# Kernel optimization log

Measured on AMD Instinct MI355X. Metric: run time of the kernel, lower is better.

## Reference

```python
import jax, jax.numpy as jnp
import numpy as np

LSTM_IN = 125
LSTM_H = 125
MLP_D_H = 512
N = 512


def _lstm_scan(x, Wih, Whh, bih, bhh):
    # x: (N, LSTM_IN); PyTorch gate order: i, f, g, o
    H = LSTM_H
    def step(carry, xt):
        h, c = carry
        g = Wih @ xt + Whh @ h + bih + bhh  # (4H,)
        i = jax.nn.sigmoid(g[:H])
        f = jax.nn.sigmoid(g[H:2 * H])
        gg = jnp.tanh(g[2 * H:3 * H])
        o = jax.nn.sigmoid(g[3 * H:])
        c = f * c + i * gg
        h = o * jnp.tanh(c)
        return (h, c), h
    init = (jnp.zeros((H,), x.dtype), jnp.zeros((H,), x.dtype))
    _, hs = jax.lax.scan(step, init, x)
    return hs  # (N, H)


def setup_inputs() -> dict:
    key = jax.random.key(0)
    ks = jax.random.split(key, 14)
    s = 0.05
    d = {
        "sentence_emb": jax.random.normal(ks[0], (N, 1, LSTM_IN), jnp.float32),
        "Wih_f": jax.random.normal(ks[1], (4 * LSTM_H, LSTM_IN), jnp.float32) * s,
        "Whh_f": jax.random.normal(ks[2], (4 * LSTM_H, LSTM_H), jnp.float32) * s,
        "bih_f": jax.random.normal(ks[3], (4 * LSTM_H,), jnp.float32) * s,
        "bhh_f": jax.random.normal(ks[4], (4 * LSTM_H,), jnp.float32) * s,
        "Wih_b": jax.random.normal(ks[5], (4 * LSTM_H, LSTM_IN), jnp.float32) * s,
        "Whh_b": jax.random.normal(ks[6], (4 * LSTM_H, LSTM_H), jnp.float32) * s,
        "bih_b": jax.random.normal(ks[7], (4 * LSTM_H,), jnp.float32) * s,
        "bhh_b": jax.random.normal(ks[8], (4 * LSTM_H,), jnp.float32) * s,
        "W1": jax.random.normal(ks[9], (MLP_D_H, 4 * LSTM_H), jnp.float32) * s,
        "b1": jax.random.normal(ks[10], (MLP_D_H,), jnp.float32) * s,
        "W2": jax.random.normal(ks[11], (1, MLP_D_H), jnp.float32) * s,
        "b2": jax.random.normal(ks[12], (1,), jnp.float32) * s,
    }
    return d


def reference(sentence_emb, Wih_f, Whh_f, bih_f, bhh_f, Wih_b, Whh_b, bih_b, bhh_b, W1, b1, W2, b2):
    x = sentence_emb[:, 0, :]  # (N, 125), batch=1
    h_fwd = _lstm_scan(x, Wih_f, Whh_f, bih_f, bhh_f)           # (N, 125)
    h_bwd = _lstm_scan(x[::-1], Wih_b, Whh_b, bih_b, bhh_b)[::-1]  # (N, 125)
    h = jnp.concatenate([h_fwd, h_bwd], axis=-1)  # (N, 250)
    # output_mtx[i, j] = MLP(concat(h[j], h[i]))
    # Decompose first linear: W1 @ cat(h_j, h_i) = Wa @ h_j + Wb @ h_i
    D = h.shape[-1]
    Pa = h @ W1[:, :D].T   # (N, H): contribution of h_j
    Pb = h @ W1[:, D:].T   # (N, H): contribution of h_i
    hidden = jnp.tanh(Pb[:, None, :] + Pa[None, :, :] + b1)  # (N, N, H)
    out = hidden @ W2[0] + b2[0]  # (N, N)
    return out
```

## Files before the change

kernel.cpp:

```cpp
#include <hip/hip_runtime.h>

typedef __bf16 bf16_t;
typedef __bf16 bf16x8 __attribute__((ext_vector_type(8)));
typedef float f32x4 __attribute__((ext_vector_type(4)));
typedef int   int4v __attribute__((ext_vector_type(4)));

#define LOG2E 1.4426950408889634f

template<int CTRL>
__device__ __forceinline__ float qperm(float x) {
  return __builtin_bit_cast(float,
      __builtin_amdgcn_update_dpp(0, __builtin_bit_cast(int, x), CTRL, 0xF, 0xF, true));
}

__device__ __forceinline__ void lds_barrier() {
  asm volatile("s_waitcnt lgkmcnt(0)\n\ts_barrier" ::: "memory");
}

__global__ __launch_bounds__(256) void pre_kernel(
    const float* __restrict__ x,
    const float* __restrict__ Wih_f, const float* __restrict__ bih_f,
    const float* __restrict__ bhh_f,
    const float* __restrict__ Wih_b, const float* __restrict__ bih_b,
    const float* __restrict__ bhh_b,
    float* __restrict__ preT)
{
  const int dir = blockIdx.x >> 5;
  const int T   = blockIdx.x & 31;
  const float* __restrict__ Wih = dir ? Wih_b : Wih_f;
  const float* __restrict__ bih = dir ? bih_b : bih_f;
  const float* __restrict__ bhh = dir ? bhh_b : bhh_f;

  const int tid = threadIdx.x;
  const int wv  = tid >> 6;
  const int lane = tid & 63;
  const int q = lane >> 4, cc = lane & 15;

  const int r  = 16 * T + cc;
  const int na = r >> 2, pa = r & 3;
  const bool vld = (na < 125);
  const float* __restrict__ Wr = Wih + (vld ? (125 * pa + na) * 125 : 0);

  bf16x8 whi[4], wlo[4];
  #pragma unroll
  for (int ks = 0; ks < 4; ++ks) {
    #pragma unroll
    for (int j = 0; j < 8; ++j) {
      int k = 32 * ks + 8 * q + j;
      float wvv = (vld && k < 125) ? Wr[k] : 0.0f;
      bf16_t hi = (bf16_t)wvv;
      whi[ks][j] = hi;
      wlo[ks][j] = (bf16_t)(wvv - (float)hi);
    }
  }

  float bias[4];
  #pragma unroll
  for (int reg = 0; reg < 4; ++reg) {
    int ro = 16 * T + 4 * q + reg;
    int no = ro >> 2, po = ro & 3;
    bias[reg] = (no < 125) ? (bih[125 * po + no] + bhh[125 * po + no]) : 0.0f;
  }

  for (int i = 0; i < 8; ++i) {
    const int tt = 8 * wv + i;
    const int t  = 16 * tt + cc;
    const int trow = dir ? (511 - t) : t;
    const float* __restrict__ xr = x + trow * 125;

    f32x4 acc = (f32x4)0.0f;
    #pragma unroll
    for (int ks = 0; ks < 4; ++ks) {
      bf16x8 xhi, xlo;
      #pragma unroll
      for (int j = 0; j < 8; ++j) {
        int k = 32 * ks + 8 * q + j;
        float xv = (k < 125) ? xr[k] : 0.0f;
        bf16_t hi = (bf16_t)xv;
        xhi[j] = hi;
        xlo[j] = (bf16_t)(xv - (float)hi);
      }
      acc = __builtin_amdgcn_mfma_f32_16x16x32_bf16(whi[ks], xhi, acc, 0, 0, 0);
      acc = __builtin_amdgcn_mfma_f32_16x16x32_bf16(whi[ks], xlo, acc, 0, 0, 0);
      acc = __builtin_amdgcn_mfma_f32_16x16x32_bf16(wlo[ks], xhi, acc, 0, 0, 0);
    }
    #pragma unroll
    for (int reg = 0; reg < 4; ++reg) {
      int ro = 16 * T + 4 * q + reg;
      preT[dir * 262144 + ro * 512 + 16 * tt + cc] = acc[reg] + bias[reg];
    }
  }
}

__global__ __launch_bounds__(512) void lstm_kernel(
    const float* __restrict__ Whh_f, const float* __restrict__ Whh_b,
    const float* __restrict__ pre,
    bf16_t* __restrict__ h_all)
{
  const int tid  = threadIdx.x;

  if (blockIdx.x >= 2) {
    const unsigned long long t0 = __builtin_amdgcn_s_memrealtime();
    float a = 1.0f + (float)tid;
    const float b = 1.0000001f;
    for (;;) {
      #pragma unroll
      for (int it = 0; it < 1024; ++it) a = fmaf(a, b, 1e-7f);
      if (__builtin_amdgcn_s_memrealtime() - t0 > 12000ull) break;
    }
    asm volatile("" :: "v"(a));
    return;
  }

  const int dir = blockIdx.x;
  const float* __restrict__ Whh = dir ? Whh_b : Whh_f;

  const int lane = tid & 63;
  const int w    = tid >> 6;
  const int q    = lane >> 4;
  const int cc   = lane & 15;
  const int lt   = cc >> 2;
  const int p    = cc & 3;

  float wm = 0.0f;
  #pragma unroll
  for (int LT = 0; LT < 4; ++LT) {
    int rr = 16 * (4 * w + LT) + cc;
    int nn = rr >> 2, pp = rr & 3;
    if (nn < 125) {
      const float* __restrict__ Wrow = Whh + (125 * pp + nn) * 125;
      #pragma unroll
      for (int ks = 0; ks < 2; ++ks)
        #pragma unroll
        for (int jj = 0; jj < 16; ++jj) {
          int k = 64 * ks + 16 * q + jj;
          if (k < 125) wm = fmaxf(wm, fabsf(Wrow[k]));
        }
    }
  }
  #pragma unroll
  for (int off = 1; off < 64; off <<= 1)
    wm = fmaxf(wm, __shfl_xor(wm, off));
  __shared__ float wmx[8];
  if (lane == 0) wmx[w] = wm;
  __syncthreads();
  float wmax = wmx[0];
  #pragma unroll
  for (int u = 1; u < 8; ++u) wmax = fmaxf(wmax, wmx[u]);
  const float s_w  = 127.0f / wmax;
  const float invq = wmax / (127.0f * 127.0f);

  int4v afrag[4][2];
  #pragma unroll
  for (int LT = 0; LT < 4; ++LT) {
    int rr = 16 * (4 * w + LT) + cc;
    int nn = rr >> 2, pp = rr & 3;
    bool avld = (nn < 125);
    const float* __restrict__ Wrow = Whh + (avld ? (125 * pp + nn) * 125 : 0);
    #pragma unroll
    for (int ks = 0; ks < 2; ++ks) {
      int4v v;
      #pragma unroll
      for (int word = 0; word < 4; ++word) {
        int b = 0;
        #pragma unroll
        for (int byte = 0; byte < 4; ++byte) {
          int jj = 4 * word + byte;
          int k  = 64 * ks + 16 * q + jj;
          int qv = 0;
          if (avld && k < 125)
            qv = (int)__builtin_rintf(Wrow[k] * s_w);
          b |= (qv & 0xFF) << (8 * byte);
        }
        v[word] = b;
      }
      afrag[LT][ks] = v;
    }
  }

  __shared__ __align__(16) char hbuf[2][128];
  if (tid < 256) hbuf[tid >> 7][tid & 127] = 0;
  if (dir == 0) {
    #pragma unroll
    for (int u = 0; u < 6; ++u) h_all[tid * 256 + 250 + u] = (bf16_t)0.0f;
  }
  __syncthreads();

  const int   r_lane = 64 * w + 16 * lt + 4 * q + p;
  const int   nset   = 16 * w + 4 * lt + q;
  const float mult   = (p == 2) ? (-2.0f * LOG2E) : (-LOG2E);
  const float sA     = (p == 2) ? 2.0f : 1.0f;
  const float sB     = (p == 2) ? -1.0f : 0.0f;
  const float dscale = mult * invq;
  const float* __restrict__ preR = pre + dir * 262144 + r_lane * 512;
  float c = 0.0f;

  float4 pv_cur = *(const float4*)preR;

  for (int g = 0; g < 128; ++g) {
    float4 pv_nxt = make_float4(0.f, 0.f, 0.f, 0.f);
    if (g < 127) pv_nxt = *(const float4*)(preR + 4 * (g + 1));

    #pragma unroll
    for (int s4 = 0; s4 < 4; ++s4) {
      const int step = 4 * g + s4;
      const int cur  = s4 & 1, nxt = cur ^ 1;
      const float pv = (s4 == 0) ? pv_cur.x : (s4 == 1) ? pv_cur.y
                     : (s4 == 2) ? pv_cur.z : pv_cur.w;
      const float pvm = mult * pv;

      int4v b0 = *(const int4v*)&hbuf[cur][16 * q];
      int4v b1 = *(const int4v*)&hbuf[cur][64 + 16 * q];

      int4v acc[4];
      #pragma unroll
      for (int LT = 0; LT < 4; ++LT) {
        int4v a = (int4v)0;
        a = __builtin_amdgcn_mfma_i32_16x16x64_i8(afrag[LT][0], b0, a, 0, 0, 0);
        a = __builtin_amdgcn_mfma_i32_16x16x64_i8(afrag[LT][1], b1, a, 0, 0, 0);
        acc[LT] = a;
      }

      int gl[4];
      #pragma unroll
      for (int LT = 0; LT < 4; ++LT) {
        int a01 = (p & 1) ? acc[LT][1] : acc[LT][0];
        int a23 = (p & 1) ? acc[LT][3] : acc[LT][2];
        gl[LT] = (p & 2) ? a23 : a01;
      }
      int b01 = (lt & 1) ? gl[1] : gl[0];
      int b23 = (lt & 1) ? gl[3] : gl[2];
      int gsel = (lt & 2) ? b23 : b01;

      float gf  = (float)gsel;
      float xg  = fmaf(gf, dscale, pvm);
      float e   = __builtin_amdgcn_exp2f(xg);
      float y   = __builtin_amdgcn_rcpf(1.0f + e);
      float act = fmaf(y, sA, sB);

      float b_i = qperm<0x00>(act);
      float b_f = qperm<0x55>(act);
      float b_g = qperm<0xAA>(act);
      float b_o = qperm<0xFF>(act);
      c = fmaf(b_f, c, b_i * b_g);
      float e2 = __builtin_amdgcn_exp2f(-2.0f * LOG2E * c);
      float tc = fmaf(__builtin_amdgcn_rcpf(1.0f + e2), 2.0f, -1.0f);
      float h  = b_o * tc;

      if (p == 0) {
        int qh = (int)__builtin_rintf(h * 127.0f);
        hbuf[nxt][nset] = (char)qh;
        if (nset < 125) {
          int t_orig = dir ? (511 - step) : step;
          h_all[t_orig * 256 + dir * 125 + nset] = (bf16_t)h;
        }
      }
      lds_barrier();
    }
    pv_cur = pv_nxt;
  }
}

__global__ __launch_bounds__(256) void qgemm_kernel(
    const bf16_t* __restrict__ h_all,
    const float* __restrict__ W1,
    const float* __restrict__ b1,
    float* __restrict__ Ea,
    float* __restrict__ Eb)
{
  const int tid  = threadIdx.x;
  const int wv   = tid >> 6;
  const int lane = tid & 63;
  const int q    = lane >> 4, cc = lane & 15;
  const int bj   = blockIdx.x & 31;
  const int bm   = blockIdx.x >> 5;
  const int m    = bm * 64 + wv * 16 + cc;
  const int j0   = bj * 16;
  const int jA   = j0 + cc;

  const bool isB = (m >= 512);
  const int  row = isB ? (m - 512) : m;
  const int  cof = isB ? 250 : 0;

  f32x4 acc = (f32x4)0.0f;
  #pragma unroll
  for (int ks = 0; ks < 8; ++ks) {
    int kb = 32 * ks + 8 * q;
    bf16x8 a = *(const bf16x8*)&h_all[jA * 256 + kb];
    bf16x8 b;
    #pragma unroll
    for (int jj = 0; jj < 8; ++jj) {
      int k = kb + jj;
      float v = (k < 250) ? W1[row * 500 + cof + k] : 0.0f;
      b[jj] = (bf16_t)v;
    }
    acc = __builtin_amdgcn_mfma_f32_16x16x32_bf16(a, b, acc, 0, 0, 0);
  }

  const float C2 = 2.0f * LOG2E;
  #pragma unroll
  for (int reg = 0; reg < 4; ++reg) {
    int j = j0 + 4 * q + reg;
    float v = acc[reg];
    if (!isB) Ea[j * 512 + m] = __builtin_amdgcn_exp2f(C2 * v);
    else      Eb[j * 512 + (m - 512)] =
                  __builtin_amdgcn_exp2f(C2 * (v + b1[m - 512]));
  }
}

__global__ __launch_bounds__(256) void outer_kernel(
    const float* __restrict__ Ea, const float* __restrict__ Eb,
    const float* __restrict__ W2, const float* __restrict__ b2,
    float* __restrict__ out)
{
  __shared__ float sa2[2][32][36];
  __shared__ float sb2[2][16][36];
  __shared__ float sw[2][32];

  const int tid = threadIdx.x;
  const int bi  = blockIdx.x >> 4;
  const int bjx = blockIdx.x & 15;
  const int i0  = bi * 16, j0 = bjx * 32;
  const int ii  = tid & 15;
  const int jj2 = tid >> 4;

  const int lj  = tid & 31, lk4 = (tid >> 5) * 4;
  const int li  = tid & 15, lk4b = ((tid >> 4) & 7) * 4;

  float accR0 = 0.0f, accR1 = 0.0f;
  float wsum = 0.0f;

  for (int kc = 0; kc < 16; ++kc) {
    const int buf = kc & 1;
    const int k0  = kc * 32;
    float4 va = *(const float4*)&Ea[(j0 + lj) * 512 + k0 + lk4];
    *(float4*)&sa2[buf][lj][lk4] = va;
    if (tid < 128) {
      float4 vb = *(const float4*)&Eb[(i0 + li) * 512 + k0 + lk4b];
      *(float4*)&sb2[buf][li][lk4b] = vb;
    }
    if (tid < 32) sw[buf][tid] = W2[k0 + tid];
    __syncthreads();

    #pragma unroll 4
    for (int kk = 0; kk < 32; kk += 2) {
      float2 wv = *(const float2*)&sw[buf][kk];
      float2 bv = *(const float2*)&sb2[buf][ii][kk];
      float2 a0 = *(const float2*)&sa2[buf][2 * jj2 + 0][kk];
      float2 a1 = *(const float2*)&sa2[buf][2 * jj2 + 1][kk];
      wsum += wv.x + wv.y;
      {
        float t1  = fmaf(a0.x, bv.x, 1.0f);
        float t2  = fmaf(a0.y, bv.y, 1.0f);
        float den = t1 * t2;
        float num = fmaf(wv.x, t2, wv.y * t1);
        accR0 = fmaf(num, __builtin_amdgcn_rcpf(den), accR0);
      }
      {
        float t1  = fmaf(a1.x, bv.x, 1.0f);
        float t2  = fmaf(a1.y, bv.y, 1.0f);
        float den = t1 * t2;
        float num = fmaf(wv.x, t2, wv.y * t1);
        accR1 = fmaf(num, __builtin_amdgcn_rcpf(den), accR1);
      }
    }
  }

  const float bb = b2[0];
  float2 o;
  o.x = wsum - 2.0f * accR0 + bb;
  o.y = wsum - 2.0f * accR1 + bb;
  *(float2*)&out[(i0 + ii) * 512 + j0 + 2 * jj2] = o;
}

extern "C" void kernel_launch(void* const* d_in, const int* in_sizes, int n_in,
                              void* d_out, int out_size, void* d_ws, size_t ws_size,
                              hipStream_t stream) {
  const float* emb   = (const float*)d_in[0];
  const float* Wih_f = (const float*)d_in[1];
  const float* Whh_f = (const float*)d_in[2];
  const float* bih_f = (const float*)d_in[3];
  const float* bhh_f = (const float*)d_in[4];
  const float* Wih_b = (const float*)d_in[5];
  const float* Whh_b = (const float*)d_in[6];
  const float* bih_b = (const float*)d_in[7];
  const float* bhh_b = (const float*)d_in[8];
  const float* W1    = (const float*)d_in[9];
  const float* b1    = (const float*)d_in[10];
  const float* W2    = (const float*)d_in[11];
  const float* b2    = (const float*)d_in[12];
  float* out = (float*)d_out;

  char* ws = (char*)d_ws;
  float*    pre   = (float*)ws;
  bf16_t*   h_all = (bf16_t*)(ws + 2 * 1024 * 1024);
  float*    Ea    = (float*)(ws + 2 * 1024 * 1024 + 256 * 1024);
  float*    Eb    = Ea + 512 * 512;

  pre_kernel<<<64, 256, 0, stream>>>(emb, Wih_f, bih_f, bhh_f,
                                     Wih_b, bih_b, bhh_b, pre);
  lstm_kernel<<<256, 512, 0, stream>>>(Whh_f, Whh_b, pre, h_all);
  qgemm_kernel<<<512, 256, 0, stream>>>(h_all, W1, b1, Ea, Eb);
  outer_kernel<<<512, 256, 0, stream>>>(Ea, Eb, W2, b2, out);
}
```

Baseline: 319.9 us.

## Drop spinning filler blocks, split LSTM MFMA chains, vectorize W1 loads

Launches the LSTM kernel with only the two working blocks and removes the 254 blocks that burned ALU cycles for about 12000 realtime ticks (likely there to keep clocks up). Each gate's two dependent int8 MFMAs become two independent MFMAs whose outputs are selected separately and summed, which shortens the per-step dependency chain in the serial recurrence. The qgemm kernel loads W1 rows as float2 where the block fits inside the valid range. The filler blocks may have been holding the GPU at a higher clock, so removing them could lengthen the latency-bound recurrence.

New measurement: 396.9 us. 1.24x slower.

```diff
diff --git a/kernel.cpp b/kernel.cpp
--- a/kernel.cpp
+++ b/kernel.cpp
@@ -15,6 +15,19 @@
 
 __device__ __forceinline__ void lds_barrier() {
   asm volatile("s_waitcnt lgkmcnt(0)\n\ts_barrier" ::: "memory");
+}
+
+__device__ __forceinline__ int dsel(const int4v a[4], int p, int lt) {
+  int gl[4];
+  #pragma unroll
+  for (int LT = 0; LT < 4; ++LT) {
+    int a01 = (p & 1) ? a[LT][1] : a[LT][0];
+    int a23 = (p & 1) ? a[LT][3] : a[LT][2];
+    gl[LT] = (p & 2) ? a23 : a01;
+  }
+  int b01 = (lt & 1) ? gl[1] : gl[0];
+  int b23 = (lt & 1) ? gl[3] : gl[2];
+  return (lt & 2) ? b23 : b01;
 }
 
 __global__ __launch_bounds__(256) void pre_kernel(
@@ -97,24 +110,10 @@
     const float* __restrict__ pre,
     bf16_t* __restrict__ h_all)
 {
-  const int tid  = threadIdx.x;
-
-  if (blockIdx.x >= 2) {
-    const unsigned long long t0 = __builtin_amdgcn_s_memrealtime();
-    float a = 1.0f + (float)tid;
-    const float b = 1.0000001f;
-    for (;;) {
-      #pragma unroll
-      for (int it = 0; it < 1024; ++it) a = fmaf(a, b, 1e-7f);
-      if (__builtin_amdgcn_s_memrealtime() - t0 > 12000ull) break;
-    }
-    asm volatile("" :: "v"(a));
-    return;
-  }
-
   const int dir = blockIdx.x;
   const float* __restrict__ Whh = dir ? Whh_b : Whh_f;
 
+  const int tid  = threadIdx.x;
   const int lane = tid & 63;
   const int w    = tid >> 6;
   const int q    = lane >> 4;
@@ -212,25 +211,15 @@
       int4v b0 = *(const int4v*)&hbuf[cur][16 * q];
       int4v b1 = *(const int4v*)&hbuf[cur][64 + 16 * q];
 
-      int4v acc[4];
+      int4v acc0[4], acc1[4];
       #pragma unroll
       for (int LT = 0; LT < 4; ++LT) {
-        int4v a = (int4v)0;
-        a = __builtin_amdgcn_mfma_i32_16x16x64_i8(afrag[LT][0], b0, a, 0, 0, 0);
-        a = __builtin_amdgcn_mfma_i32_16x16x64_i8(afrag[LT][1], b1, a, 0, 0, 0);
-        acc[LT] = a;
-      }
-
-      int gl[4];
-      #pragma unroll
-      for (int LT = 0; LT < 4; ++LT) {
-        int a01 = (p & 1) ? acc[LT][1] : acc[LT][0];
-        int a23 = (p & 1) ? acc[LT][3] : acc[LT][2];
-        gl[LT] = (p & 2) ? a23 : a01;
-      }
-      int b01 = (lt & 1) ? gl[1] : gl[0];
-      int b23 = (lt & 1) ? gl[3] : gl[2];
-      int gsel = (lt & 2) ? b23 : b01;
+        acc0[LT] = __builtin_amdgcn_mfma_i32_16x16x64_i8(
+                       afrag[LT][0], b0, (int4v)0, 0, 0, 0);
+        acc1[LT] = __builtin_amdgcn_mfma_i32_16x16x64_i8(
+                       afrag[LT][1], b1, (int4v)0, 0, 0, 0);
+      }
+      const int gsel = dsel(acc0, p, lt) + dsel(acc1, p, lt);
 
       float gf  = (float)gsel;
       float xg  = fmaf(gf, dscale, pvm);
@@ -281,6 +270,7 @@
   const bool isB = (m >= 512);
   const int  row = isB ? (m - 512) : m;
   const int  cof = isB ? 250 : 0;
+  const float* __restrict__ Wrow = W1 + row * 500 + cof;
 
   f32x4 acc = (f32x4)0.0f;
   #pragma unroll
@@ -288,11 +278,20 @@
     int kb = 32 * ks + 8 * q;
     bf16x8 a = *(const bf16x8*)&h_all[jA * 256 + kb];
     bf16x8 b;
-    #pragma unroll
-    for (int jj = 0; jj < 8; ++jj) {
-      int k = kb + jj;
-      float v = (k < 250) ? W1[row * 500 + cof + k] : 0.0f;
-      b[jj] = (bf16_t)v;
+    if (kb + 8 <= 250) {
+      const float2* __restrict__ Wp = (const float2*)(Wrow + kb);
+      #pragma unroll
+      for (int jj = 0; jj < 4; ++jj) {
+        float2 v = Wp[jj];
+        b[2 * jj + 0] = (bf16_t)v.x;
+        b[2 * jj + 1] = (bf16_t)v.y;
+      }
+    } else {
+      #pragma unroll
+      for (int jj = 0; jj < 8; ++jj) {
+        int k = kb + jj;
+        b[jj] = (bf16_t)((k < 250) ? Wrow[k] : 0.0f);
+      }
     }
     acc = __builtin_amdgcn_mfma_f32_16x16x32_bf16(a, b, acc, 0, 0, 0);
   }
@@ -399,7 +398,7 @@
 
   pre_kernel<<<64, 256, 0, stream>>>(emb, Wih_f, bih_f, bhh_f,
                                      Wih_b, bih_b, bhh_b, pre);
-  lstm_kernel<<<256, 512, 0, stream>>>(Whh_f, Whh_b, pre, h_all);
+  lstm_kernel<<<2, 512, 0, stream>>>(Whh_f, Whh_b, pre, h_all);
   qgemm_kernel<<<512, 256, 0, stream>>>(h_all, W1, b1, Ea, Eb);
   outer_kernel<<<512, 256, 0, stream>>>(Ea, Eb, W2, b2, out);
 }
```
